# Optimization experiments

Hardware: AMD Instinct MI355X
Metric: run time of the kernel (lower is better)

Reference implementation:

```python
import jax, jax.numpy as jnp
import numpy as np

IM = 64      # im_size
B = 256      # number of latent elements
P = 2        # num_primitives
S = 2        # max_num_shapes
HID = 64     # mlp hidden width


def setup_inputs() -> dict:
    key = jax.random.key(0)
    ks = jax.random.split(key, 8)

    def lin_w(k, fan_in, fan_out):
        # small-ish init so exp(mlp_out) stays finite
        return (jax.random.normal(k, (P, fan_in, fan_out), dtype=jnp.float32)
                / np.float32(np.sqrt(fan_in)))

    return {
        "program_id": jax.random.randint(ks[0], (B,), 0, 3),
        "shape_ids": jax.random.randint(ks[1], (B, S), 0, P),
        "raw_positions": jax.random.normal(ks[2], (B, S, 2), dtype=jnp.float32),
        "w0": lin_w(ks[3], 1, HID),   "b0": jnp.zeros((P, HID), jnp.float32),
        "w1": lin_w(ks[4], HID, HID), "b1": jnp.zeros((P, HID), jnp.float32),
        "w2": lin_w(ks[5], HID, HID), "b2": jnp.zeros((P, HID), jnp.float32),
        "w3": lin_w(ks[6], HID, 1),   "b3": jnp.zeros((P, 1), jnp.float32),
        "logit_multipliers_raw": jnp.ones((P,), jnp.float32),
    }


def reference(program_id, shape_ids, raw_positions,
              w0, b0, w1, b1, w2, b2, w3, b3, logit_multipliers_raw):
    im = IM
    # canvas grid in [-1, 1]
    lin = jnp.linspace(-1.0, 1.0, im, dtype=raw_positions.dtype)
    cx, cy = jnp.meshgrid(lin, lin, indexing="xy")  # [im, im]

    pos = jax.nn.sigmoid(raw_positions) - 0.5  # [B, S, 2]
    dx = cx[None, None] - pos[..., 0][..., None, None]  # [B, S, im, im]
    dy = cy[None, None] - pos[..., 1][..., None, None]

    theta = jnp.arctan2(dy, dx).reshape(B, S, im * im, 1)  # mlp input

    def g(p):
        return p[shape_ids]  # gather per-(element, slot) primitive params

    h = jax.nn.relu(jnp.einsum("bsni,bsio->bsno", theta, g(w0)) + g(b0)[:, :, None, :])
    h = jax.nn.relu(jnp.einsum("bsni,bsio->bsno", h, g(w1)) + g(b1)[:, :, None, :])
    h = jax.nn.relu(jnp.einsum("bsni,bsio->bsno", h, g(w2)) + g(b2)[:, :, None, :])
    o = (jnp.einsum("bsni,bsio->bsno", h, g(w3)) + g(b3)[:, :, None, :]).reshape(B, S, im, im)

    mult = jnp.exp(logit_multipliers_raw)[shape_ids][..., None, None]  # [B, S, 1, 1]
    logits = mult * (jnp.exp(o) - jnp.sqrt(dx * dx + dy * dy))
    probs = jax.nn.sigmoid(logits)  # [B, S, im, im]

    p0, p1 = probs[:, 0], probs[:, 1]
    pid = program_id[:, None, None]
    combined = jnp.clip(jnp.where(pid == 2, p0 - p1, p0 + p1), 0.0, 1.0)
    return jnp.where(pid == 0, p0, combined)  # [B, im, im]
```

## Files before the change

### kernel.cpp

```cpp
#include <hip/hip_runtime.h>
#include <math.h>

#define IM 64
#define NBATCH 256
#define HID 64
#define TT 2048
#define PI_F 3.14159265358979f

typedef _Float16 f16;
typedef _Float16 f16x8 __attribute__((ext_vector_type(8)));
typedef _Float16 f16x2 __attribute__((ext_vector_type(2)));
typedef float    f32x4 __attribute__((ext_vector_type(4)));
typedef float    f32x2 __attribute__((ext_vector_type(2)));


static __device__ __forceinline__ f16x2 cvt2(float a, float b) {
    return __builtin_bit_cast(f16x2, __builtin_amdgcn_cvt_pkrtz(a, b));
}
static __device__ __forceinline__ f32x2 pmax2(f32x2 v) {
    return __builtin_elementwise_max(v, (f32x2)0.f);
}
static __device__ __forceinline__ f16x2 hmax2(f16x2 v) {
    return __builtin_elementwise_max(v, (f16x2)(_Float16)0.f);
}
static __device__ __forceinline__ float fast_atan2(float y, float x) {
    float ax = fabsf(x), ay = fabsf(y);
    float mx = fmaxf(ax, ay), mn = fminf(ax, ay);
    float t = mn * __builtin_amdgcn_rcpf(mx);
    float z = t * t;
    float p = fmaf(z, -0.01172120f, 0.05265332f);
    p = fmaf(z, p, -0.11643287f);
    p = fmaf(z, p,  0.19354346f);
    p = fmaf(z, p, -0.33262347f);
    p = fmaf(z, p,  0.99997726f);
    float r = t * p;
    r = (ay > ax)  ? 1.5707964f - r : r;
    r = (x < 0.f)  ? 3.1415927f - r : r;
    return (y < 0.f) ? -r : r;
}

__global__ __launch_bounds__(256) void setup_kernel(
    const float* __restrict__ w0, const float* __restrict__ b0,
    const float* __restrict__ w1, const float* __restrict__ b1,
    const float* __restrict__ w2, const float* __restrict__ b2,
    const float* __restrict__ w3, const float* __restrict__ b3,
    const int*   __restrict__ shape_ids,
    const float* __restrict__ raw_positions,
    const float* __restrict__ lmr,
    float* __restrict__ wsf)
{
    const int tid = threadIdx.x;
    if (blockIdx.x >= 16) {
        #pragma unroll
        for (int rep = 0; rep < 8; ++rep) {
            int idx = rep*256 + tid;
            int e = idx >> 2, c = idx & 3;
            float v;
            if (c == 0)      v = 1.f/(1.f + __expf(-raw_positions[e*2+0])) - 0.5f;
            else if (c == 1) v = 1.f/(1.f + __expf(-raw_positions[e*2+1])) - 0.5f;
            else if (c == 2) v = __expf(lmr[shape_ids[e]]);
            else             v = (float)shape_ids[e];
            wsf[8320 + idx] = v;
        }
        return;
    }

    const int wave = tid >> 6;
    const int lane = tid & 63;
    const int u = lane & 15, g = lane >> 4;
    const int chunk = blockIdx.x*4 + wave;
    const int pg = chunk >> 5;
    const int i0 = (chunk & 31)*64 + lane;
    const float theta = -PI_F + (2.0f*PI_F/(float)(TT-1)) * (float)i0;

    f16x8 wfA[4][2], wfB[4][2];
    #pragma unroll
    for (int mt = 0; mt < 4; ++mt)
        #pragma unroll
        for (int kh = 0; kh < 2; ++kh) {
            f16x8 a, bq;
            #pragma unroll
            for (int j = 0; j < 8; ++j) {
                const int k1 = 32*kh + 8*g + j;
                const int k2 = 32*kh + 16*(j>>2) + 4*g + (j&3);
                a[j]  = (f16)w1[pg*4096 + k1*64 + 16*mt + u];
                bq[j] = (f16)w2[pg*4096 + k2*64 + 16*mt + u];
            }
            wfA[mt][kh] = a; wfB[mt][kh] = bq;
        }
    f16x8 w0r[2], b0r[2];
    #pragma unroll
    for (int kh = 0; kh < 2; ++kh) {
        f16x8 a, bq;
        #pragma unroll
        for (int j = 0; j < 8; ++j) {
            a[j]  = (f16)w0[pg*64 + 32*kh + 8*g + j];
            bq[j] = (f16)b0[pg*64 + 32*kh + 8*g + j];
        }
        w0r[kh] = a; b0r[kh] = bq;
    }
    f32x4 bv1[4], bv2[4], w3v[4];
    #pragma unroll
    for (int mt = 0; mt < 4; ++mt) {
        bv1[mt] = *(const f32x4*)&b1[pg*64 + 16*mt + 4*g];
        bv2[mt] = *(const f32x4*)&b2[pg*64 + 16*mt + 4*g];
        w3v[mt] = *(const f32x4*)&w3[pg*64 + 16*mt + 4*g];
    }

    float th[4];
    #pragma unroll
    for (int nt = 0; nt < 4; ++nt) th[nt] = __shfl(theta, 16*nt + u);

    f16x8 bf[4][2];
    #pragma unroll
    for (int nt = 0; nt < 4; ++nt) {
        const f16 thh = (f16)th[nt];
        const f16x2 th2 = {thh, thh};
        #pragma unroll
        for (int kh = 0; kh < 2; ++kh) {
            union { f16x2 h2[4]; f16x8 v8; } uu;
            union { f16x8 v8; f16x2 h2[4]; } wv, bv_;
            wv.v8 = w0r[kh]; bv_.v8 = b0r[kh];
            #pragma unroll
            for (int q = 0; q < 4; ++q)
                uu.h2[q] = hmax2(__builtin_elementwise_fma(th2, wv.h2[q], bv_.h2[q]));
            bf[nt][kh] = uu.v8;
        }
    }

    f16x8 cf[4][2];
    #pragma unroll
    for (int mp = 0; mp < 2; ++mp) {
        f32x4 acc[2][4];
        #pragma unroll
        for (int mh = 0; mh < 2; ++mh) {
            const int mt = 2*mp + mh;
            #pragma unroll
            for (int nt = 0; nt < 4; ++nt) {
                f32x4 a = __builtin_amdgcn_mfma_f32_16x16x32_f16(wfA[mt][0], bf[nt][0], bv1[mt], 0,0,0);
                a = __builtin_amdgcn_mfma_f32_16x16x32_f16(wfA[mt][1], bf[nt][1], a, 0,0,0);
                acc[mh][nt] = a;
            }
        }
        #pragma unroll
        for (int nt = 0; nt < 4; ++nt) {
            union { f16x2 h2[4]; f16x8 v8; } uu;
            #pragma unroll
            for (int hh = 0; hh < 2; ++hh) {
                const f32x4 av = acc[hh][nt];
                uu.h2[hh*2+0] = hmax2(cvt2(av[0], av[1]));
                uu.h2[hh*2+1] = hmax2(cvt2(av[2], av[3]));
            }
            cf[nt][mp] = uu.v8;
        }
    }

    f32x2 hp2[4] = {{0.f,0.f},{0.f,0.f},{0.f,0.f},{0.f,0.f}};
    #pragma unroll
    for (int mt = 0; mt < 4; ++mt) {
        const f32x2 w301 = {w3v[mt][0], w3v[mt][1]}, w323 = {w3v[mt][2], w3v[mt][3]};
        #pragma unroll
        for (int nt = 0; nt < 4; ++nt) {
            f32x4 a = __builtin_amdgcn_mfma_f32_16x16x32_f16(wfB[mt][0], cf[nt][0], bv2[mt], 0,0,0);
            a = __builtin_amdgcn_mfma_f32_16x16x32_f16(wfB[mt][1], cf[nt][1], a, 0,0,0);
            f32x2 e01 = pmax2((f32x2){a[0], a[1]});
            f32x2 e23 = pmax2((f32x2){a[2], a[3]});
            hp2[nt] = e01*w301 + hp2[nt];
            hp2[nt] = e23*w323 + hp2[nt];
        }
    }
    float hp[4];
    #pragma unroll
    for (int nt = 0; nt < 4; ++nt) {
        hp[nt] = hp2[nt][0] + hp2[nt][1];
        hp[nt] += __shfl_xor(hp[nt], 16);
        hp[nt] += __shfl_xor(hp[nt], 32);
    }
    float ov = hp[0];
    if (g == 1) ov = hp[1];
    if (g == 2) ov = hp[2];
    if (g == 3) ov = hp[3];

    wsf[10752 + pg*TT + i0] = ov + b3[pg];
}

__global__ __launch_bounds__(256) void render_kernel(
    const int* __restrict__ program_id,
    const float* __restrict__ wsf,
    float* __restrict__ out)
{
    const float* tab = wsf + 10752;
    const int gi = blockIdx.x * 256 + threadIdx.x;
    const int b    = gi >> 10;
    const int p4   = gi & 1023;
    const int row  = p4 >> 4;
    const int col0 = (p4 & 15) << 2;
    const float cy = -1.f + (2.f/63.f)*(float)row;

    const f32x4 scv0 = *(const f32x4*)&wsf[8320 + (b*2 + 0)*4];
    const f32x4 scv1 = *(const f32x4*)&wsf[8320 + (b*2 + 1)*4];
    const int   pid  = program_id[b];

    f32x4 res;
    #pragma unroll
    for (int k = 0; k < 4; ++k) {
        const float cx = -1.f + (2.f/63.f)*(float)(col0 + k);
        float p01[2];
        #pragma unroll
        for (int s = 0; s < 2; ++s) {
            const f32x4 scv = s ? scv1 : scv0;
            const float dx = cx - scv[0], dy = cy - scv[1];
            const float theta = fast_atan2(dy, dx);
            const float r2 = sqrtf(dx*dx + dy*dy);
            float x = (theta + PI_F) * ((float)(TT-1)/(2.f*PI_F));
            x = fminf(fmaxf(x, 0.f), (float)(TT-1));
            const float fi = floorf(fminf(x, (float)(TT-2)));
            const int   i  = (int)fi;
            const float f  = x - fi;
            const float* tb = tab + ((int)scv[3])*TT;
            const float t0 = tb[i], t1 = tb[i+1];
            const float o  = fmaf(f, t1 - t0, t0);
            const float logit = scv[2] * (__expf(o) - r2);
            p01[s] = __builtin_amdgcn_rcpf(1.f + __expf(-logit));
        }
        float r;
        if (pid == 0) {
            r = p01[0];
        } else {
            float c = (pid == 2) ? (p01[0] - p01[1]) : (p01[0] + p01[1]);
            r = fminf(fmaxf(c, 0.f), 1.f);
        }
        res[k] = r;
    }
    *(f32x4*)&out[b*(IM*IM) + row*64 + col0] = res;
}

extern "C" void kernel_launch(void* const* d_in, const int* in_sizes, int n_in,
                              void* d_out, int out_size, void* d_ws, size_t ws_size,
                              hipStream_t stream) {
    const int*   program_id    = (const int*)  d_in[0];
    const int*   shape_ids     = (const int*)  d_in[1];
    const float* raw_positions = (const float*)d_in[2];
    const float* w0            = (const float*)d_in[3];
    const float* b0            = (const float*)d_in[4];
    const float* w1            = (const float*)d_in[5];
    const float* b1            = (const float*)d_in[6];
    const float* w2            = (const float*)d_in[7];
    const float* b2            = (const float*)d_in[8];
    const float* w3            = (const float*)d_in[9];
    const float* b3            = (const float*)d_in[10];
    const float* lmr           = (const float*)d_in[11];
    float* out = (float*)d_out;
    float* wsf = (float*)d_ws;

    setup_kernel<<<17, 256, 0, stream>>>(w0, b0, w1, b1, w2, b2, w3, b3,
                                         shape_ids, raw_positions, lmr, wsf);

    render_kernel<<<1024, 256, 0, stream>>>(program_id, wsf, out);
}
```

Before: 18.29 us.

## Stage MLP weights in LDS and move per-element setup into render kernel

After: 16.23 us. -11.3%, faster.

```diff
diff --git a/kernel.cpp b/kernel.cpp
--- a/kernel.cpp
+++ b/kernel.cpp
@@ -9,6 +9,7 @@
 
 typedef _Float16 f16;
 typedef _Float16 f16x8 __attribute__((ext_vector_type(8)));
+typedef _Float16 f16x4 __attribute__((ext_vector_type(4)));
 typedef _Float16 f16x2 __attribute__((ext_vector_type(2)));
 typedef float    f32x4 __attribute__((ext_vector_type(4)));
 typedef float    f32x2 __attribute__((ext_vector_type(2)));
@@ -44,32 +45,41 @@
     const float* __restrict__ w1, const float* __restrict__ b1,
     const float* __restrict__ w2, const float* __restrict__ b2,
     const float* __restrict__ w3, const float* __restrict__ b3,
-    const int*   __restrict__ shape_ids,
-    const float* __restrict__ raw_positions,
-    const float* __restrict__ lmr,
     float* __restrict__ wsf)
 {
+    __shared__ alignas(16) f16  W1[4096];
+    __shared__ alignas(16) f16  W2[4096];
+    __shared__ alignas(16) f16  w0s[64], b0s[64];
+    __shared__ alignas(16) float b1s[64], b2s[64], w3s[64];
+
     const int tid = threadIdx.x;
-    if (blockIdx.x >= 16) {
-        #pragma unroll
-        for (int rep = 0; rep < 8; ++rep) {
-            int idx = rep*256 + tid;
-            int e = idx >> 2, c = idx & 3;
-            float v;
-            if (c == 0)      v = 1.f/(1.f + __expf(-raw_positions[e*2+0])) - 0.5f;
-            else if (c == 1) v = 1.f/(1.f + __expf(-raw_positions[e*2+1])) - 0.5f;
-            else if (c == 2) v = __expf(lmr[shape_ids[e]]);
-            else             v = (float)shape_ids[e];
-            wsf[8320 + idx] = v;
-        }
-        return;
-    }
+    const int blk = blockIdx.x;
+    const int pg  = blk >> 3;
+
+    {
+        const f32x4* s1 = (const f32x4*)(w1 + pg*4096);
+        const f32x4* s2 = (const f32x4*)(w2 + pg*4096);
+        #pragma unroll
+        for (int r = 0; r < 4; ++r) {
+            const int i4 = r*256 + tid;
+            const f32x4 v1 = s1[i4], v2 = s2[i4];
+            ((f16x4*)W1)[i4] = (f16x4){(f16)v1[0], (f16)v1[1], (f16)v1[2], (f16)v1[3]};
+            ((f16x4*)W2)[i4] = (f16x4){(f16)v2[0], (f16)v2[1], (f16)v2[2], (f16)v2[3]};
+        }
+        if (tid < 64) {
+            w0s[tid] = (f16)w0[pg*64 + tid];
+            b0s[tid] = (f16)b0[pg*64 + tid];
+            b1s[tid] = b1[pg*64 + tid];
+            b2s[tid] = b2[pg*64 + tid];
+            w3s[tid] = w3[pg*64 + tid];
+        }
+    }
+    __syncthreads();
 
     const int wave = tid >> 6;
     const int lane = tid & 63;
     const int u = lane & 15, g = lane >> 4;
-    const int chunk = blockIdx.x*4 + wave;
-    const int pg = chunk >> 5;
+    const int chunk = blk*4 + wave;
     const int i0 = (chunk & 31)*64 + lane;
     const float theta = -PI_F + (2.0f*PI_F/(float)(TT-1)) * (float)i0;
 
@@ -83,28 +93,23 @@
             for (int j = 0; j < 8; ++j) {
                 const int k1 = 32*kh + 8*g + j;
                 const int k2 = 32*kh + 16*(j>>2) + 4*g + (j&3);
-                a[j]  = (f16)w1[pg*4096 + k1*64 + 16*mt + u];
-                bq[j] = (f16)w2[pg*4096 + k2*64 + 16*mt + u];
+                a[j]  = W1[k1*64 + 16*mt + u];
+                bq[j] = W2[k2*64 + 16*mt + u];
             }
             wfA[mt][kh] = a; wfB[mt][kh] = bq;
         }
     f16x8 w0r[2], b0r[2];
     #pragma unroll
     for (int kh = 0; kh < 2; ++kh) {
-        f16x8 a, bq;
-        #pragma unroll
-        for (int j = 0; j < 8; ++j) {
-            a[j]  = (f16)w0[pg*64 + 32*kh + 8*g + j];
-            bq[j] = (f16)b0[pg*64 + 32*kh + 8*g + j];
-        }
-        w0r[kh] = a; b0r[kh] = bq;
+        w0r[kh] = *(const f16x8*)&w0s[32*kh + 8*g];
+        b0r[kh] = *(const f16x8*)&b0s[32*kh + 8*g];
     }
     f32x4 bv1[4], bv2[4], w3v[4];
     #pragma unroll
     for (int mt = 0; mt < 4; ++mt) {
-        bv1[mt] = *(const f32x4*)&b1[pg*64 + 16*mt + 4*g];
-        bv2[mt] = *(const f32x4*)&b2[pg*64 + 16*mt + 4*g];
-        w3v[mt] = *(const f32x4*)&w3[pg*64 + 16*mt + 4*g];
+        bv1[mt] = *(const f32x4*)&b1s[16*mt + 4*g];
+        bv2[mt] = *(const f32x4*)&b2s[16*mt + 4*g];
+        w3v[mt] = *(const f32x4*)&w3s[16*mt + 4*g];
     }
 
     float th[4];
@@ -181,25 +186,37 @@
     if (g == 2) ov = hp[2];
     if (g == 3) ov = hp[3];
 
-    wsf[10752 + pg*TT + i0] = ov + b3[pg];
+    wsf[pg*TT + i0] = ov + b3[pg];
 }
 
 __global__ __launch_bounds__(256) void render_kernel(
-    const int* __restrict__ program_id,
+    const int*   __restrict__ program_id,
+    const int*   __restrict__ shape_ids,
+    const float* __restrict__ raw_positions,
+    const float* __restrict__ lmr,
     const float* __restrict__ wsf,
     float* __restrict__ out)
 {
-    const float* tab = wsf + 10752;
-    const int gi = blockIdx.x * 256 + threadIdx.x;
-    const int b    = gi >> 10;
-    const int p4   = gi & 1023;
-    const int row  = p4 >> 4;
-    const int col0 = (p4 & 15) << 2;
+    const int blk = blockIdx.x;
+    const int b   = blk >> 2;
+    const int q4  = blk & 3;
+    const int tid = threadIdx.x;
+
+    const int pid = program_id[b];
+    const int pg0 = shape_ids[b*2 + 0];
+    const int pg1 = shape_ids[b*2 + 1];
+    const float posx0 = 1.f/(1.f + __expf(-raw_positions[b*4+0])) - 0.5f;
+    const float posy0 = 1.f/(1.f + __expf(-raw_positions[b*4+1])) - 0.5f;
+    const float posx1 = 1.f/(1.f + __expf(-raw_positions[b*4+2])) - 0.5f;
+    const float posy1 = 1.f/(1.f + __expf(-raw_positions[b*4+3])) - 0.5f;
+    const float mult0 = __expf(lmr[pg0]);
+    const float mult1 = __expf(lmr[pg1]);
+    const float* tb0 = wsf + pg0*TT;
+    const float* tb1 = wsf + pg1*TT;
+
+    const int px0  = q4*1024 + tid*4;
+    const int row  = px0 >> 6, col0 = px0 & 63;
     const float cy = -1.f + (2.f/63.f)*(float)row;
-
-    const f32x4 scv0 = *(const f32x4*)&wsf[8320 + (b*2 + 0)*4];
-    const f32x4 scv1 = *(const f32x4*)&wsf[8320 + (b*2 + 1)*4];
-    const int   pid  = program_id[b];
 
     f32x4 res;
     #pragma unroll
@@ -208,8 +225,11 @@
         float p01[2];
         #pragma unroll
         for (int s = 0; s < 2; ++s) {
-            const f32x4 scv = s ? scv1 : scv0;
-            const float dx = cx - scv[0], dy = cy - scv[1];
+            const float px = s ? posx1 : posx0;
+            const float py = s ? posy1 : posy0;
+            const float mu = s ? mult1 : mult0;
+            const float* tb = s ? tb1 : tb0;
+            const float dx = cx - px, dy = cy - py;
             const float theta = fast_atan2(dy, dx);
             const float r2 = sqrtf(dx*dx + dy*dy);
             float x = (theta + PI_F) * ((float)(TT-1)/(2.f*PI_F));
@@ -217,10 +237,9 @@
             const float fi = floorf(fminf(x, (float)(TT-2)));
             const int   i  = (int)fi;
             const float f  = x - fi;
-            const float* tb = tab + ((int)scv[3])*TT;
             const float t0 = tb[i], t1 = tb[i+1];
             const float o  = fmaf(f, t1 - t0, t0);
-            const float logit = scv[2] * (__expf(o) - r2);
+            const float logit = mu * (__expf(o) - r2);
             p01[s] = __builtin_amdgcn_rcpf(1.f + __expf(-logit));
         }
         float r;
@@ -232,7 +251,7 @@
         }
         res[k] = r;
     }
-    *(f32x4*)&out[b*(IM*IM) + row*64 + col0] = res;
+    *(f32x4*)&out[b*(IM*IM) + px0] = res;
 }
 
 extern "C" void kernel_launch(void* const* d_in, const int* in_sizes, int n_in,
@@ -253,8 +272,8 @@
     float* out = (float*)d_out;
     float* wsf = (float*)d_ws;
 
-    setup_kernel<<<17, 256, 0, stream>>>(w0, b0, w1, b1, w2, b2, w3, b3,
-                                         shape_ids, raw_positions, lmr, wsf);
-
-    render_kernel<<<1024, 256, 0, stream>>>(program_id, wsf, out);
-}
+    setup_kernel<<<16, 256, 0, stream>>>(w0, b0, w1, b1, w2, b2, w3, b3, wsf);
+
+    render_kernel<<<1024, 256, 0, stream>>>(program_id, shape_ids,
+                                            raw_positions, lmr, wsf, out);
+}
```
